# Kernel optimization log

Measured on AMD Instinct MI355X. Metric: run time of the kernel, lower is better.

Reference implementation:

```python
import jax, jax.numpy as jnp
import numpy as np

D_MODEL = 1024
NUM_HEADS = 16
HEAD_DIM = D_MODEL // NUM_HEADS


def setup_inputs() -> dict:
    key = jax.random.key(0)
    kx, kq, kk, kv, ko = jax.random.split(key, 5)
    B, S = 2, 2048
    scale = 1.0 / np.sqrt(D_MODEL)
    return {
        "x": jax.random.normal(kx, (B, S, D_MODEL), dtype=jnp.float32),
        "W_q": jax.random.normal(kq, (D_MODEL, D_MODEL), dtype=jnp.float32) * scale,
        "W_k": jax.random.normal(kk, (D_MODEL, D_MODEL), dtype=jnp.float32) * scale,
        "W_v": jax.random.normal(kv, (D_MODEL, D_MODEL), dtype=jnp.float32) * scale,
        "W_o": jax.random.normal(ko, (D_MODEL, D_MODEL), dtype=jnp.float32) * scale,
        "causal": 1,
    }


def _attn(x, W_q, W_k, W_v, W_o, causal):
    B, S, D = x.shape
    H, Hd = NUM_HEADS, HEAD_DIM
    # projections: nn.Linear applies x @ W.T
    q = (x @ W_q.T).reshape(B, S, H, Hd)
    k = (x @ W_k.T).reshape(B, S, H, Hd)
    v = (x @ W_v.T).reshape(B, S, H, Hd)
    # scores: [B, H, S, S]
    scores = jnp.einsum("bqhd,bkhd->bhqk", q, k) / np.sqrt(Hd)
    if causal:
        mask = jnp.triu(jnp.ones((S, S), dtype=bool), k=1)
        scores = jnp.where(mask, -jnp.inf, scores)
    attn = jax.nn.softmax(scores, axis=-1)
    out = jnp.einsum("bhqk,bkhd->bqhd", attn, v).reshape(B, S, D)
    return out @ W_o.T


def reference(x, W_q, W_k, W_v, W_o, causal):
    return _attn(x, W_q, W_k, W_v, W_o, causal)
```

## Files before the change

kernel.cpp:

```cpp
#include <hip/hip_runtime.h>

typedef __attribute__((ext_vector_type(8))) short bf16x8;
typedef __attribute__((ext_vector_type(4))) float f32x4;
typedef __attribute__((ext_vector_type(4))) unsigned short u16x4;

#define MFMA16(a, b, c) __builtin_amdgcn_mfma_f32_16x16x32_bf16((a), (b), (c), 0, 0, 0)

static constexpr int D_MODEL = 1024;
static constexpr int SEQ = 2048;
static constexpr int NH = 16;
static constexpr int HD = 64;
static constexpr int LDA = 40;
static constexpr int MST = 136;
static constexpr float NEG_BIG = -1.0e30f;

__device__ __forceinline__ unsigned short f2bf(float f) {
  union { float f; unsigned int u; } v; v.f = f;
  unsigned int r = v.u + 0x7fffu + ((v.u >> 16) & 1u);
  return (unsigned short)(r >> 16);
}

__device__ __forceinline__ unsigned int cvtpk_bf16(float a, float b) {
  unsigned int r;
  asm("v_cvt_pk_bf16_f32 %0, %1, %2" : "=v"(r) : "v"(a), "v"(b));
  return r;
}

__device__ __forceinline__ bf16x8 ld8(const void* p, size_t eidx, int bf) {
  if (bf) return *(const bf16x8*)((const unsigned short*)p + eidx);
  const float* f = (const float*)p + eidx;
  f32x4 lo = *(const f32x4*)f;
  f32x4 hi = *(const f32x4*)(f + 4);
  bf16x8 r;
  r[0] = (short)f2bf(lo[0]); r[1] = (short)f2bf(lo[1]);
  r[2] = (short)f2bf(lo[2]); r[3] = (short)f2bf(lo[3]);
  r[4] = (short)f2bf(hi[0]); r[5] = (short)f2bf(hi[1]);
  r[6] = (short)f2bf(hi[2]); r[7] = (short)f2bf(hi[3]);
  return r;
}

__device__ __forceinline__ void async16(const unsigned short* g, unsigned short* l) {
  __builtin_amdgcn_global_load_lds(
      (const __attribute__((address_space(1))) void*)g,
      (__attribute__((address_space(3))) void*)l, 16, 0, 0);
}

__global__ __launch_bounds__(64) void detect_kernel(
    const unsigned short* __restrict__ xs, int* __restrict__ flag) {
  int lane = threadIdx.x;
  unsigned short s = xs[2 * lane];
  int e = (s >> 7) & 0xFF;
  bool hit = (e >= 117 && e <= 129);
  unsigned long long m = __ballot(hit);
  if (lane == 0) { flag[0] = (__popcll(m) >= 32) ? 1 : 0; flag[1] = 1; }
}

__global__ __launch_bounds__(256) void convert_kernel(
    const void* __restrict__ X,
    const void* __restrict__ W0, const void* __restrict__ W1,
    const void* __restrict__ W2, const void* __restrict__ W3,
    const int* __restrict__ flag,
    unsigned short* __restrict__ Xb, unsigned short* __restrict__ Wb)
{
  const int bf = *flag;
  const int ty = blockIdx.y;
  const void* src; unsigned short* dst; size_t n;
  if (ty == 0) { src = X; dst = Xb; n = (size_t)2 * SEQ * D_MODEL; }
  else {
    src = (ty == 1) ? W0 : (ty == 2) ? W1 : (ty == 3) ? W2 : W3;
    dst = Wb + (size_t)(ty - 1) * D_MODEL * D_MODEL;
    n = (size_t)D_MODEL * D_MODEL;
  }
  size_t i = ((size_t)blockIdx.x * 256 + threadIdx.x) * 8;
  if (i >= n) return;
  *(bf16x8*)(dst + i) = ld8(src, i, bf);
}

__device__ __forceinline__ void gemm_fast_core(
    const unsigned short* __restrict__ A, const unsigned short* __restrict__ B,
    int tm, int tn, unsigned short* As, unsigned short* Bs, f32x4 acc[4][4])
{
  const int t = threadIdx.x;
  const int lane = t & 63;
  const int w = t >> 6;
  const int wm = (w >> 1) * 64, wn = (w & 1) * 64;
  const int quad = lane >> 4, l16 = lane & 15;
  const int srow = lane >> 3;
  const int scol = ((lane & 7) ^ srow) * 8;
  const int xa = l16 & 7;

#pragma unroll
  for (int mi = 0; mi < 4; ++mi)
#pragma unroll
    for (int ni = 0; ni < 4; ++ni)
      acc[mi][ni] = (f32x4){0.f, 0.f, 0.f, 0.f};

  for (int k0 = 0; k0 < D_MODEL; k0 += 64) {
    __syncthreads();
#pragma unroll
    for (int j = 0; j < 4; ++j) {
      const int row = w * 32 + j * 8;
      async16(A + (size_t)(tm + row + srow) * D_MODEL + k0 + scol, As + row * 64);
      async16(B + (size_t)(tn + row + srow) * D_MODEL + k0 + scol, Bs + row * 64);
    }
    asm volatile("s_waitcnt vmcnt(0)" ::: "memory");
    __syncthreads();
    bf16x8 af[2][4], bfv[2][4];
#pragma unroll
    for (int ks = 0; ks < 2; ++ks) {
#pragma unroll
      for (int mi = 0; mi < 4; ++mi)
        af[ks][mi] = *(const bf16x8*)(As + (wm + mi * 16 + l16) * 64 +
                                      ((ks * 4 + quad) ^ xa) * 8);
#pragma unroll
      for (int ni = 0; ni < 4; ++ni)
        bfv[ks][ni] = *(const bf16x8*)(Bs + (wn + ni * 16 + l16) * 64 +
                                       ((ks * 4 + quad) ^ xa) * 8);
    }
#pragma unroll
    for (int ks = 0; ks < 2; ++ks)
#pragma unroll
      for (int mi = 0; mi < 4; ++mi)
#pragma unroll
        for (int ni = 0; ni < 4; ++ni)
          acc[mi][ni] = MFMA16(af[ks][mi], bfv[ks][ni], acc[mi][ni]);
  }
}

__global__ __launch_bounds__(256) void qkv_fast_kernel(
    const unsigned short* __restrict__ X,
    const unsigned short* __restrict__ Wb,
    unsigned short* __restrict__ qd,
    unsigned short* __restrict__ kws,
    unsigned short* __restrict__ vws)
{
  __shared__ __align__(16) unsigned short smem[2 * 128 * 64];
  unsigned short* As = smem;
  unsigned short* Bs = smem + 128 * 64;
  const int bid = blockIdx.x;
  const int xcd = bid & 7, s0 = bid >> 3;
  const int tmg = xcd >> 2, tng = xcd & 3;
  const int tm_local = s0 / 6, zt = s0 % 6;
  const int z = zt >> 1, tn_local = zt & 1;
  const int tm = (tmg * 16 + tm_local) * 128;
  const int tn = (tng * 2 + tn_local) * 128;
  const unsigned short* W = Wb + (size_t)z * D_MODEL * D_MODEL;
  f32x4 acc[4][4];
  gemm_fast_core(X, W, tm, tn, As, Bs, acc);

  const int t = threadIdx.x;
  const int lane = t & 63, w = t >> 6;
  const int wm = (w >> 1) * 64, wn = (w & 1) * 64;
  const int quad = lane >> 4, l16 = lane & 15;

  if (z == 2) {
    const int b = tm >> 11;
    const int sb = tm & 2047;
#pragma unroll
    for (int ph = 0; ph < 2; ++ph) {
      __syncthreads();
      if ((w & 1) == ph) {
#pragma unroll
        for (int mi = 0; mi < 4; ++mi)
#pragma unroll
          for (int ni = 0; ni < 4; ++ni)
#pragma unroll
            for (int r = 0; r < 4; ++r) {
              int m_local = wm + mi * 16 + quad * 4 + r;
              int n_sub = ni * 16 + l16;
              smem[n_sub * MST + m_local] = f2bf(acc[mi][ni][r]);
            }
      }
      __syncthreads();
      const int row = t >> 2, c0 = (t & 3) * 32;
      const int n_g = tn + ph * 64 + row;
      const int h = n_g >> 6, d = n_g & 63;
      unsigned short* dst = vws + (((size_t)b * NH + h) * HD + d) * SEQ + sb + c0;
#pragma unroll
      for (int cc = 0; cc < 4; ++cc)
        *(bf16x8*)(dst + cc * 8) = *(const bf16x8*)(smem + row * MST + c0 + cc * 8);
    }
    return;
  }
#pragma unroll
  for (int mi = 0; mi < 4; ++mi)
#pragma unroll
    for (int ni = 0; ni < 4; ++ni)
#pragma unroll
      for (int r = 0; r < 4; ++r) {
        int m = tm + wm + mi * 16 + quad * 4 + r;
        int n = tn + wn + ni * 16 + l16;
        unsigned short bv = f2bf(acc[mi][ni][r]);
        if (z == 0) {
          qd[(size_t)m * D_MODEL + n] = bv;
        } else {
          int b = m >> 11, sg = m & 2047;
          int h = n >> 6, d = n & 63;
          kws[(((size_t)b * NH + h) * SEQ + sg) * HD + d] = bv;
        }
      }
}

__global__ __launch_bounds__(256) void oproj_fast_kernel(
    const unsigned short* __restrict__ AW,
    const unsigned short* __restrict__ Wo,
    float* __restrict__ tmp)
{
  __shared__ __align__(16) unsigned short As[128 * 64];
  __shared__ __align__(16) unsigned short Bs[128 * 64];
  const int bid = blockIdx.x;
  const int xcd = bid & 7, s0 = bid >> 3;
  const int tmg = xcd >> 2, tng = xcd & 3;
  const int tm = (tmg * 16 + (s0 >> 1)) * 128;
  const int tn = (tng * 2 + (s0 & 1)) * 128;
  f32x4 acc[4][4];
  gemm_fast_core(AW, Wo, tm, tn, As, Bs, acc);

  const int t = threadIdx.x;
  const int lane = t & 63, w = t >> 6;
  const int wm = (w >> 1) * 64, wn = (w & 1) * 64;
  const int quad = lane >> 4, l16 = lane & 15;
#pragma unroll
  for (int mi = 0; mi < 4; ++mi)
#pragma unroll
    for (int ni = 0; ni < 4; ++ni)
#pragma unroll
      for (int r = 0; r < 4; ++r) {
        int m = tm + wm + mi * 16 + quad * 4 + r;
        int n = tn + wn + ni * 16 + l16;
        tmp[(size_t)m * D_MODEL + n] = acc[mi][ni][r];
      }
}

__device__ __forceinline__ void gemm_tile_128x128(
    const void* __restrict__ A, const void* __restrict__ B, int bf,
    int tm, int tn, unsigned short* As, unsigned short* Bs, f32x4 acc[4][4])
{
  const int t = threadIdx.x;
  const int lane = t & 63;
  const int w = t >> 6;
  const int wm = (w >> 1) * 64, wn = (w & 1) * 64;
  const int quad = lane >> 4, l16 = lane & 15;
  const int r0 = t >> 2, kc = (t & 3) * 8;
  const int r1 = r0 + 64;

#pragma unroll
  for (int mi = 0; mi < 4; ++mi)
#pragma unroll
    for (int ni = 0; ni < 4; ++ni)
      acc[mi][ni] = (f32x4){0.f, 0.f, 0.f, 0.f};

  for (int k0 = 0; k0 < D_MODEL; k0 += 32) {
    bf16x8 a0 = ld8(A, (size_t)(tm + r0) * D_MODEL + k0 + kc, bf);
    bf16x8 a1 = ld8(A, (size_t)(tm + r1) * D_MODEL + k0 + kc, bf);
    bf16x8 b0 = ld8(B, (size_t)(tn + r0) * D_MODEL + k0 + kc, bf);
    bf16x8 b1 = ld8(B, (size_t)(tn + r1) * D_MODEL + k0 + kc, bf);
    __syncthreads();
    *(bf16x8*)(As + r0 * LDA + kc) = a0;
    *(bf16x8*)(As + r1 * LDA + kc) = a1;
    *(bf16x8*)(Bs + r0 * LDA + kc) = b0;
    *(bf16x8*)(Bs + r1 * LDA + kc) = b1;
    __syncthreads();
    bf16x8 af[4], bfv[4];
#pragma unroll
    for (int mi = 0; mi < 4; ++mi)
      af[mi] = *(const bf16x8*)(As + (wm + mi * 16 + l16) * LDA + quad * 8);
#pragma unroll
    for (int ni = 0; ni < 4; ++ni)
      bfv[ni] = *(const bf16x8*)(Bs + (wn + ni * 16 + l16) * LDA + quad * 8);
#pragma unroll
    for (int mi = 0; mi < 4; ++mi)
#pragma unroll
      for (int ni = 0; ni < 4; ++ni)
        acc[mi][ni] = MFMA16(af[mi], bfv[ni], acc[mi][ni]);
  }
}

__global__ __launch_bounds__(256) void qkv_kernel(
    const void* __restrict__ X,
    const void* __restrict__ Wq,
    const void* __restrict__ Wk,
    const void* __restrict__ Wv,
    const int* __restrict__ flag,
    unsigned short* __restrict__ qd,
    unsigned short* __restrict__ kws,
    unsigned short* __restrict__ vws)
{
  __shared__ __align__(16) unsigned short As[128 * LDA];
  __shared__ __align__(16) unsigned short Bs[128 * LDA];
  const int bf = *flag;
  const int z = blockIdx.z;
  const void* W = (z == 0) ? Wq : ((z == 1) ? Wk : Wv);
  const int tm = blockIdx.y * 128, tn = blockIdx.x * 128;
  f32x4 acc[4][4];
  gemm_tile_128x128(X, W, bf, tm, tn, As, Bs, acc);

  const int t = threadIdx.x;
  const int lane = t & 63, w = t >> 6;
  const int wm = (w >> 1) * 64, wn = (w & 1) * 64;
  const int quad = lane >> 4, l16 = lane & 15;
#pragma unroll
  for (int mi = 0; mi < 4; ++mi)
#pragma unroll
    for (int ni = 0; ni < 4; ++ni)
#pragma unroll
      for (int r = 0; r < 4; ++r) {
        int m = tm + wm + mi * 16 + quad * 4 + r;
        int n = tn + wn + ni * 16 + l16;
        unsigned short bv = f2bf(acc[mi][ni][r]);
        if (z == 0) {
          qd[(size_t)m * D_MODEL + n] = bv;
        } else {
          int b = m >> 11, s = m & 2047;
          int h = n >> 6, d = n & 63;
          if (z == 1) kws[(((size_t)b * NH + h) * SEQ + s) * HD + d] = bv;
          else        vws[(((size_t)b * NH + h) * HD + d) * SEQ + s] = bv;
        }
      }
}

__global__ __launch_bounds__(256) void oproj_kernel(
    const unsigned short* __restrict__ AW,
    const void* __restrict__ Wo,
    const int* __restrict__ flag,
    float* __restrict__ tmp)
{
  __shared__ __align__(16) unsigned short As[128 * LDA];
  __shared__ __align__(16) unsigned short Bs[128 * LDA];
  const int bf = *flag;
  const int t = threadIdx.x;
  const int lane = t & 63;
  const int w = t >> 6;
  const int wm = (w >> 1) * 64, wn = (w & 1) * 64;
  const int quad = lane >> 4, l16 = lane & 15;
  const int r0 = t >> 2, kc = (t & 3) * 8;
  const int r1 = r0 + 64;
  const int tm = blockIdx.y * 128, tn = blockIdx.x * 128;
  f32x4 acc[4][4];
#pragma unroll
  for (int mi = 0; mi < 4; ++mi)
#pragma unroll
    for (int ni = 0; ni < 4; ++ni)
      acc[mi][ni] = (f32x4){0.f, 0.f, 0.f, 0.f};

  for (int k0 = 0; k0 < D_MODEL; k0 += 32) {
    bf16x8 a0 = *(const bf16x8*)(AW + (size_t)(tm + r0) * D_MODEL + k0 + kc);
    bf16x8 a1 = *(const bf16x8*)(AW + (size_t)(tm + r1) * D_MODEL + k0 + kc);
    bf16x8 b0 = ld8(Wo, (size_t)(tn + r0) * D_MODEL + k0 + kc, bf);
    bf16x8 b1 = ld8(Wo, (size_t)(tn + r1) * D_MODEL + k0 + kc, bf);
    __syncthreads();
    *(bf16x8*)(As + r0 * LDA + kc) = a0;
    *(bf16x8*)(As + r1 * LDA + kc) = a1;
    *(bf16x8*)(Bs + r0 * LDA + kc) = b0;
    *(bf16x8*)(Bs + r1 * LDA + kc) = b1;
    __syncthreads();
    bf16x8 af[4], bfv[4];
#pragma unroll
    for (int mi = 0; mi < 4; ++mi)
      af[mi] = *(const bf16x8*)(As + (wm + mi * 16 + l16) * LDA + quad * 8);
#pragma unroll
    for (int ni = 0; ni < 4; ++ni)
      bfv[ni] = *(const bf16x8*)(Bs + (wn + ni * 16 + l16) * LDA + quad * 8);
#pragma unroll
    for (int mi = 0; mi < 4; ++mi)
#pragma unroll
      for (int ni = 0; ni < 4; ++ni)
        acc[mi][ni] = MFMA16(af[mi], bfv[ni], acc[mi][ni]);
  }
#pragma unroll
  for (int mi = 0; mi < 4; ++mi)
#pragma unroll
    for (int ni = 0; ni < 4; ++ni)
#pragma unroll
      for (int r = 0; r < 4; ++r) {
        int m = tm + wm + mi * 16 + quad * 4 + r;
        int n = tn + wn + ni * 16 + l16;
        tmp[(size_t)m * D_MODEL + n] = acc[mi][ni][r];
      }
}

__global__ __launch_bounds__(256) void attn_kernel(
    unsigned short* __restrict__ Qd,
    const unsigned short* __restrict__ Kb,
    const unsigned short* __restrict__ Vt,
    const int* __restrict__ causal_p)
{
  __shared__ __align__(16) unsigned short Ks[2][64 * 64];
  __shared__ __align__(16) unsigned short Vs[2][64 * 64];
  const int bid = blockIdx.x;
  const int xcd = bid & 7, slot = bid >> 3;
  const int bh = xcd * 4 + (slot >> 4);
  const int gx = slot & 15;
  const int g = (slot & 32) ? gx : (15 - gx);
  const int b = bh >> 4, h = bh & 15;
  const int t = threadIdx.x, lane = t & 63, w = t >> 6;
  const int quad = lane >> 4, l16 = lane & 15;
  const int causal = *causal_p;
  unsigned short* qh = Qd + (size_t)b * SEQ * D_MODEL + h * HD;
  const unsigned short* kh = Kb + ((size_t)b * NH + h) * SEQ * HD;
  const unsigned short* vh = Vt + ((size_t)b * NH + h) * HD * SEQ;
  const float Cs = 0.125f * 1.4426950408889634f;
  const int srow = lane >> 3;
  const int gcol = ((lane & 7) ^ srow) * 8;
  const int xa = l16 & 7;
  const int dtile = 2 * g + (w >> 1);
  const int ktend = causal ? (2 * g + 2) : (SEQ / 64);

  int kvp[2];
#pragma unroll
  for (int j2 = 0; j2 < 2; ++j2) {
    const int rp = w * 16 + j2 * 8 + srow;
    kvp[j2] = ((rp >> 4) & 1) * 32 + ((rp >> 2) & 3) * 8 + ((rp >> 5) & 1) * 4 + (rp & 3);
  }

  int q0[2];
  bf16x8 aq[2][2];
#pragma unroll
  for (int s = 0; s < 2; ++s) {
    q0[s] = g * 128 + w * 32 + s * 16;
#pragma unroll
    for (int ch = 0; ch < 2; ++ch)
      aq[s][ch] = *(const bf16x8*)(qh + (size_t)(q0[s] + l16) * D_MODEL +
                                   ch * 32 + quad * 8);
  }

  f32x4 oaccT[2][4];
#pragma unroll
  for (int s = 0; s < 2; ++s)
#pragma unroll
    for (int db = 0; db < 4; ++db) oaccT[s][db] = (f32x4){0.f, 0.f, 0.f, 0.f};
  float lsum[2] = {0.f, 0.f};

#pragma unroll
  for (int j2 = 0; j2 < 2; ++j2) {
    const int row = w * 16 + j2 * 8;
    async16(kh + (size_t)kvp[j2] * HD + gcol, &Ks[0][row * 64]);
    async16(vh + (size_t)(row + srow) * SEQ + gcol, &Vs[0][row * 64]);
  }

  for (int kt = 0; kt < ktend; ++kt) {
    const int cur = kt & 1;
    asm volatile("s_waitcnt vmcnt(0)" ::: "memory");
    __syncthreads();
    if (kt + 1 < ktend) {
      const int nxt = cur ^ 1;
#pragma unroll
      for (int j2 = 0; j2 < 2; ++j2) {
        const int row = w * 16 + j2 * 8;
        async16(kh + (size_t)((kt + 1) * 64 + kvp[j2]) * HD + gcol,
                &Ks[nxt][row * 64]);
        async16(vh + (size_t)(row + srow) * SEQ + (kt + 1) * 64 + gcol,
                &Vs[nxt][row * 64]);
      }
    }
    if (causal && kt > dtile) continue;

    bf16x8 kfr[4][2], vfr[4][2];
#pragma unroll
    for (int cb = 0; cb < 4; ++cb)
#pragma unroll
      for (int hf = 0; hf < 2; ++hf) {
        kfr[cb][hf] = *(const bf16x8*)(&Ks[cur][(cb * 16 + l16) * 64 +
                                                ((hf * 4 + quad) ^ xa) * 8]);
        vfr[cb][hf] = *(const bf16x8*)(&Vs[cur][(cb * 16 + l16) * 64 +
                                                ((hf * 4 + quad) ^ xa) * 8]);
      }
#pragma unroll
    for (int s = 0; s < 2; ++s) {
      f32x4 sc[4];
      __builtin_amdgcn_s_setprio(1);
#pragma unroll
      for (int cb = 0; cb < 4; ++cb) {
        sc[cb] = (f32x4){0.f, 0.f, 0.f, 0.f};
        sc[cb] = MFMA16(kfr[cb][0], aq[s][0], sc[cb]);
        sc[cb] = MFMA16(kfr[cb][1], aq[s][1], sc[cb]);
      }
      __builtin_amdgcn_s_setprio(0);
      if (causal && kt == dtile) {
        int q = q0[s] + l16;
#pragma unroll
        for (int cb = 0; cb < 4; ++cb)
#pragma unroll
          for (int r = 0; r < 4; ++r)
            if (kt * 64 + (cb & 1) * 32 + quad * 8 + (cb >> 1) * 4 + r > q)
              sc[cb][r] = NEG_BIG;
      }
      float ls = 0.f;
#pragma unroll
      for (int cb = 0; cb < 4; ++cb)
#pragma unroll
        for (int r = 0; r < 4; ++r) {
          float p = __builtin_amdgcn_exp2f(sc[cb][r] * Cs);
          ls += p;
          sc[cb][r] = p;
        }
      lsum[s] += ls;
      bf16x8 bp[2];
#pragma unroll
      for (int hf = 0; hf < 2; ++hf) {
        union { unsigned int w4[4]; bf16x8 v; } u;
        u.w4[0] = cvtpk_bf16(sc[hf][0], sc[hf][1]);
        u.w4[1] = cvtpk_bf16(sc[hf][2], sc[hf][3]);
        u.w4[2] = cvtpk_bf16(sc[2 + hf][0], sc[2 + hf][1]);
        u.w4[3] = cvtpk_bf16(sc[2 + hf][2], sc[2 + hf][3]);
        bp[hf] = u.v;
      }
      __builtin_amdgcn_s_setprio(1);
#pragma unroll
      for (int db = 0; db < 4; ++db) {
        oaccT[s][db] = MFMA16(vfr[db][0], bp[0], oaccT[s][db]);
        oaccT[s][db] = MFMA16(vfr[db][1], bp[1], oaccT[s][db]);
      }
      __builtin_amdgcn_s_setprio(0);
    }
  }
#pragma unroll
  for (int s = 0; s < 2; ++s) {
    float l = lsum[s];
    l += __shfl_xor(l, 16, 64);
    l += __shfl_xor(l, 32, 64);
    float inv = 1.0f / l;
#pragma unroll
    for (int db = 0; db < 4; ++db) {
      u16x4 o;
#pragma unroll
      for (int r = 0; r < 4; ++r) o[r] = f2bf(oaccT[s][db][r] * inv);
      *(u16x4*)(qh + (size_t)(q0[s] + l16) * D_MODEL + db * 16 + quad * 4) = o;
    }
  }
}

__global__ __launch_bounds__(256) void final_kernel(
    const float* __restrict__ tmp, void* __restrict__ out,
    const int* __restrict__ flag)
{
  const int bf = *flag;
  size_t i = ((size_t)blockIdx.x * 256 + threadIdx.x) * 8;
  f32x4 lo = *(const f32x4*)(tmp + i);
  f32x4 hi = *(const f32x4*)(tmp + i + 4);
  if (bf) {
    bf16x8 r;
    r[0] = (short)f2bf(lo[0]); r[1] = (short)f2bf(lo[1]);
    r[2] = (short)f2bf(lo[2]); r[3] = (short)f2bf(lo[3]);
    r[4] = (short)f2bf(hi[0]); r[5] = (short)f2bf(hi[1]);
    r[6] = (short)f2bf(hi[2]); r[7] = (short)f2bf(hi[3]);
    *(bf16x8*)((unsigned short*)out + i) = r;
  } else {
    *(f32x4*)((float*)out + i) = lo;
    *(f32x4*)((float*)out + i + 4) = hi;
  }
}

extern "C" void kernel_launch(void* const* d_in, const int* in_sizes, int n_in,
                              void* d_out, int out_size, void* d_ws, size_t ws_size,
                              hipStream_t stream) {
  const void* X  = d_in[0];
  const void* Wq = d_in[1];
  const void* Wk = d_in[2];
  const void* Wv = d_in[3];
  const void* Wo = d_in[4];
  const int* causal = (const int*)d_in[5];

  const size_t NE = (size_t)2 * SEQ * D_MODEL;
  const size_t WE = (size_t)D_MODEL * D_MODEL;
  int* flag0 = (int*)d_ws;
  int* flag1 = flag0 + 1;
  unsigned short* kws = (unsigned short*)((char*)d_ws + 64);
  unsigned short* vws = kws + NE;
  float* tmp = (float*)kws;
  unsigned short* Wb = vws + NE;
  unsigned short* qd = (unsigned short*)d_out;
  unsigned short* Xb = qd + NE;

  const bool big = ws_size >= (size_t)64 + 24ull * 1024 * 1024;

  hipLaunchKernelGGL(detect_kernel, dim3(1), dim3(64), 0, stream,
                     (const unsigned short*)X, flag0);
  if (big) {
    hipLaunchKernelGGL(convert_kernel, dim3(2048, 5), dim3(256), 0, stream,
                       X, Wq, Wk, Wv, Wo, flag0, Xb, Wb);
    hipLaunchKernelGGL(qkv_fast_kernel, dim3(768), dim3(256), 0, stream,
                       Xb, Wb, qd, kws, vws);
    hipLaunchKernelGGL(attn_kernel, dim3(512), dim3(256), 0, stream,
                       qd, kws, vws, causal);
    hipLaunchKernelGGL(oproj_fast_kernel, dim3(256), dim3(256), 0, stream,
                       qd, Wb + 3 * WE, tmp);
  } else {
    hipLaunchKernelGGL(qkv_kernel, dim3(8, 32, 3), dim3(256), 0, stream,
                       X, Wq, Wk, Wv, flag0, qd, kws, vws);
    hipLaunchKernelGGL(attn_kernel, dim3(512), dim3(256), 0, stream,
                       qd, kws, vws, causal);
    hipLaunchKernelGGL(oproj_kernel, dim3(8, 32), dim3(256), 0, stream,
                       qd, Wo, flag0, tmp);
  }
  hipLaunchKernelGGL(final_kernel, dim3(2048), dim3(256), 0, stream,
                     tmp, d_out, flag0);
}
```

Before: 212.7 us.

## Double-buffer GEMM K-loop and shrink attention blocks to 64 query rows

The shared GEMM core now prefetches the next 64-wide K slab into a second LDS buffer while the current one feeds MFMAs, and raises wave priority around the MFMA block. The attention kernel moves from 256-thread blocks over 128 query rows to 128-thread blocks over 64 query rows with twice as many blocks, which drops the per-wave causal skip logic and balances causal work with a mirrored tile order. This aims to hide global-load latency in the projections and cut wasted or idle waves in attention, at the cost of doubled GEMM LDS use and more K/V loads per query row in attention.

```diff
diff --git a/kernel.cpp b/kernel.cpp
--- a/kernel.cpp
+++ b/kernel.cpp
@@ -78,7 +78,7 @@
 
 __device__ __forceinline__ void gemm_fast_core(
     const unsigned short* __restrict__ A, const unsigned short* __restrict__ B,
-    int tm, int tn, unsigned short* As, unsigned short* Bs, f32x4 acc[4][4])
+    int tm, int tn, unsigned short* smem, f32x4 acc[4][4])
 {
   const int t = threadIdx.x;
   const int lane = t & 63;
@@ -95,28 +95,44 @@
     for (int ni = 0; ni < 4; ++ni)
       acc[mi][ni] = (f32x4){0.f, 0.f, 0.f, 0.f};
 
-  for (int k0 = 0; k0 < D_MODEL; k0 += 64) {
-    __syncthreads();
-#pragma unroll
-    for (int j = 0; j < 4; ++j) {
-      const int row = w * 32 + j * 8;
-      async16(A + (size_t)(tm + row + srow) * D_MODEL + k0 + scol, As + row * 64);
-      async16(B + (size_t)(tn + row + srow) * D_MODEL + k0 + scol, Bs + row * 64);
-    }
+#pragma unroll
+  for (int j = 0; j < 4; ++j) {
+    const int row = w * 32 + j * 8;
+    async16(A + (size_t)(tm + row + srow) * D_MODEL + scol, smem + row * 64);
+    async16(B + (size_t)(tn + row + srow) * D_MODEL + scol,
+            smem + 8192 + row * 64);
+  }
+
+  for (int kt = 0; kt < 16; ++kt) {
+    const int co = (kt & 1) << 14;
     asm volatile("s_waitcnt vmcnt(0)" ::: "memory");
     __syncthreads();
+    if (kt < 15) {
+      const int no = ((kt & 1) ^ 1) << 14;
+      const int k0 = (kt + 1) * 64;
+#pragma unroll
+      for (int j = 0; j < 4; ++j) {
+        const int row = w * 32 + j * 8;
+        async16(A + (size_t)(tm + row + srow) * D_MODEL + k0 + scol,
+                smem + no + row * 64);
+        async16(B + (size_t)(tn + row + srow) * D_MODEL + k0 + scol,
+                smem + no + 8192 + row * 64);
+      }
+    }
     bf16x8 af[2][4], bfv[2][4];
 #pragma unroll
     for (int ks = 0; ks < 2; ++ks) {
 #pragma unroll
       for (int mi = 0; mi < 4; ++mi)
-        af[ks][mi] = *(const bf16x8*)(As + (wm + mi * 16 + l16) * 64 +
+        af[ks][mi] = *(const bf16x8*)(smem + co + (wm + mi * 16 + l16) * 64 +
                                       ((ks * 4 + quad) ^ xa) * 8);
 #pragma unroll
       for (int ni = 0; ni < 4; ++ni)
-        bfv[ks][ni] = *(const bf16x8*)(Bs + (wn + ni * 16 + l16) * 64 +
+        bfv[ks][ni] = *(const bf16x8*)(smem + co + 8192 +
+                                       (wn + ni * 16 + l16) * 64 +
                                        ((ks * 4 + quad) ^ xa) * 8);
     }
+    __builtin_amdgcn_s_setprio(1);
 #pragma unroll
     for (int ks = 0; ks < 2; ++ks)
 #pragma unroll
@@ -124,6 +140,7 @@
 #pragma unroll
         for (int ni = 0; ni < 4; ++ni)
           acc[mi][ni] = MFMA16(af[ks][mi], bfv[ks][ni], acc[mi][ni]);
+    __builtin_amdgcn_s_setprio(0);
   }
 }
 
@@ -134,9 +151,7 @@
     unsigned short* __restrict__ kws,
     unsigned short* __restrict__ vws)
 {
-  __shared__ __align__(16) unsigned short smem[2 * 128 * 64];
-  unsigned short* As = smem;
-  unsigned short* Bs = smem + 128 * 64;
+  __shared__ __align__(16) unsigned short smem[4 * 128 * 64];
   const int bid = blockIdx.x;
   const int xcd = bid & 7, s0 = bid >> 3;
   const int tmg = xcd >> 2, tng = xcd & 3;
@@ -146,7 +161,7 @@
   const int tn = (tng * 2 + tn_local) * 128;
   const unsigned short* W = Wb + (size_t)z * D_MODEL * D_MODEL;
   f32x4 acc[4][4];
-  gemm_fast_core(X, W, tm, tn, As, Bs, acc);
+  gemm_fast_core(X, W, tm, tn, smem, acc);
 
   const int t = threadIdx.x;
   const int lane = t & 63, w = t >> 6;
@@ -206,15 +221,14 @@
     const unsigned short* __restrict__ Wo,
     float* __restrict__ tmp)
 {
-  __shared__ __align__(16) unsigned short As[128 * 64];
-  __shared__ __align__(16) unsigned short Bs[128 * 64];
+  __shared__ __align__(16) unsigned short smem[4 * 128 * 64];
   const int bid = blockIdx.x;
   const int xcd = bid & 7, s0 = bid >> 3;
   const int tmg = xcd >> 2, tng = xcd & 3;
   const int tm = (tmg * 16 + (s0 >> 1)) * 128;
   const int tn = (tng * 2 + (s0 & 1)) * 128;
   f32x4 acc[4][4];
-  gemm_fast_core(AW, Wo, tm, tn, As, Bs, acc);
+  gemm_fast_core(AW, Wo, tm, tn, smem, acc);
 
   const int t = threadIdx.x;
   const int lane = t & 63, w = t >> 6;
@@ -379,7 +393,7 @@
       }
 }
 
-__global__ __launch_bounds__(256) void attn_kernel(
+__global__ __launch_bounds__(128) void attn_kernel(
     unsigned short* __restrict__ Qd,
     const unsigned short* __restrict__ Kb,
     const unsigned short* __restrict__ Vt,
@@ -389,9 +403,10 @@
   __shared__ __align__(16) unsigned short Vs[2][64 * 64];
   const int bid = blockIdx.x;
   const int xcd = bid & 7, slot = bid >> 3;
-  const int bh = xcd * 4 + (slot >> 4);
-  const int gx = slot & 15;
-  const int g = (slot & 32) ? gx : (15 - gx);
+  const int q = slot >> 5;
+  const int r = slot & 31;
+  const int gg = (q & 1) ? (31 - r) : r;
+  const int bh = xcd * 4 + q;
   const int b = bh >> 4, h = bh & 15;
   const int t = threadIdx.x, lane = t & 63, w = t >> 6;
   const int quad = lane >> 4, l16 = lane & 15;
@@ -403,13 +418,12 @@
   const int srow = lane >> 3;
   const int gcol = ((lane & 7) ^ srow) * 8;
   const int xa = l16 & 7;
-  const int dtile = 2 * g + (w >> 1);
-  const int ktend = causal ? (2 * g + 2) : (SEQ / 64);
-
-  int kvp[2];
-#pragma unroll
-  for (int j2 = 0; j2 < 2; ++j2) {
-    const int rp = w * 16 + j2 * 8 + srow;
+  const int ktend = causal ? (gg + 1) : (SEQ / 64);
+
+  int kvp[4];
+#pragma unroll
+  for (int j2 = 0; j2 < 4; ++j2) {
+    const int rp = w * 32 + j2 * 8 + srow;
     kvp[j2] = ((rp >> 4) & 1) * 32 + ((rp >> 2) & 3) * 8 + ((rp >> 5) & 1) * 4 + (rp & 3);
   }
 
@@ -417,7 +431,7 @@
   bf16x8 aq[2][2];
 #pragma unroll
   for (int s = 0; s < 2; ++s) {
-    q0[s] = g * 128 + w * 32 + s * 16;
+    q0[s] = gg * 64 + w * 32 + s * 16;
 #pragma unroll
     for (int ch = 0; ch < 2; ++ch)
       aq[s][ch] = *(const bf16x8*)(qh + (size_t)(q0[s] + l16) * D_MODEL +
@@ -432,8 +446,8 @@
   float lsum[2] = {0.f, 0.f};
 
 #pragma unroll
-  for (int j2 = 0; j2 < 2; ++j2) {
-    const int row = w * 16 + j2 * 8;
+  for (int j2 = 0; j2 < 4; ++j2) {
+    const int row = w * 32 + j2 * 8;
     async16(kh + (size_t)kvp[j2] * HD + gcol, &Ks[0][row * 64]);
     async16(vh + (size_t)(row + srow) * SEQ + gcol, &Vs[0][row * 64]);
   }
@@ -445,15 +459,14 @@
     if (kt + 1 < ktend) {
       const int nxt = cur ^ 1;
 #pragma unroll
-      for (int j2 = 0; j2 < 2; ++j2) {
-        const int row = w * 16 + j2 * 8;
+      for (int j2 = 0; j2 < 4; ++j2) {
+        const int row = w * 32 + j2 * 8;
         async16(kh + (size_t)((kt + 1) * 64 + kvp[j2]) * HD + gcol,
                 &Ks[nxt][row * 64]);
         async16(vh + (size_t)(row + srow) * SEQ + (kt + 1) * 64 + gcol,
                 &Vs[nxt][row * 64]);
       }
     }
-    if (causal && kt > dtile) continue;
 
     bf16x8 kfr[4][2], vfr[4][2];
 #pragma unroll
@@ -476,23 +489,23 @@
         sc[cb] = MFMA16(kfr[cb][1], aq[s][1], sc[cb]);
       }
       __builtin_amdgcn_s_setprio(0);
-      if (causal && kt == dtile) {
-        int q = q0[s] + l16;
+      if (causal && kt == gg) {
+        int qq = q0[s] + l16;
 #pragma unroll
         for (int cb = 0; cb < 4; ++cb)
 #pragma unroll
-          for (int r = 0; r < 4; ++r)
-            if (kt * 64 + (cb & 1) * 32 + quad * 8 + (cb >> 1) * 4 + r > q)
-              sc[cb][r] = NEG_BIG;
+          for (int rr = 0; rr < 4; ++rr)
+            if (kt * 64 + (cb & 1) * 32 + quad * 8 + (cb >> 1) * 4 + rr > qq)
+              sc[cb][rr] = NEG_BIG;
       }
       float ls = 0.f;
 #pragma unroll
       for (int cb = 0; cb < 4; ++cb)
 #pragma unroll
-        for (int r = 0; r < 4; ++r) {
-          float p = __builtin_amdgcn_exp2f(sc[cb][r] * Cs);
+        for (int rr = 0; rr < 4; ++rr) {
+          float p = __builtin_amdgcn_exp2f(sc[cb][rr] * Cs);
           ls += p;
-          sc[cb][r] = p;
+          sc[cb][rr] = p;
         }
       lsum[s] += ls;
       bf16x8 bp[2];
@@ -524,7 +537,7 @@
     for (int db = 0; db < 4; ++db) {
       u16x4 o;
 #pragma unroll
-      for (int r = 0; r < 4; ++r) o[r] = f2bf(oaccT[s][db][r] * inv);
+      for (int rr = 0; rr < 4; ++rr) o[rr] = f2bf(oaccT[s][db][rr] * inv);
       *(u16x4*)(qh + (size_t)(q0[s] + l16) * D_MODEL + db * 16 + quad * 4) = o;
     }
   }
@@ -581,14 +594,14 @@
                        X, Wq, Wk, Wv, Wo, flag0, Xb, Wb);
     hipLaunchKernelGGL(qkv_fast_kernel, dim3(768), dim3(256), 0, stream,
                        Xb, Wb, qd, kws, vws);
-    hipLaunchKernelGGL(attn_kernel, dim3(512), dim3(256), 0, stream,
+    hipLaunchKernelGGL(attn_kernel, dim3(1024), dim3(128), 0, stream,
                        qd, kws, vws, causal);
     hipLaunchKernelGGL(oproj_fast_kernel, dim3(256), dim3(256), 0, stream,
                        qd, Wb + 3 * WE, tmp);
   } else {
     hipLaunchKernelGGL(qkv_kernel, dim3(8, 32, 3), dim3(256), 0, stream,
                        X, Wq, Wk, Wv, flag0, qd, kws, vws);
-    hipLaunchKernelGGL(attn_kernel, dim3(512), dim3(256), 0, stream,
+    hipLaunchKernelGGL(attn_kernel, dim3(1024), dim3(128), 0, stream,
                        qd, kws, vws, causal);
     hipLaunchKernelGGL(oproj_kernel, dim3(8, 32), dim3(256), 0, stream,
                        qd, Wo, flag0, tmp);
```

After: 202.1 us. -5.0%, faster.
